# Kernel tuning notes

Measured on AMD Instinct MI355X. Metric: run time of the kernel, lower is better.

The kernel has to match this reference:

```python
import jax, jax.numpy as jnp
import numpy as np

T, D, H, E = 8192, 1024, 2048, 8


def setup_inputs() -> dict:
    key = jax.random.key(0)
    k1, k2, k3 = jax.random.split(key, 3)
    x = jax.random.normal(k1, (T, D), dtype=jnp.float32)
    # counts must sum to T; use a uniform split (reference handles any valid split)
    num_tokens_per_expert = jnp.full((E,), T // E, dtype=jnp.int32)
    w_up = jax.random.normal(k2, (E, H, D), dtype=jnp.float32) * (1.0 / np.sqrt(D))
    w_down = jax.random.normal(k3, (E, D, H), dtype=jnp.float32) * (1.0 / np.sqrt(H))
    return {"x": x, "num_tokens_per_expert": num_tokens_per_expert, "w_up": w_up, "w_down": w_down}


def reference(x, num_tokens_per_expert, w_up, w_down):
    """Grouped MoE expert MLP: per-expert  x @ w_up[e].T -> relu^2 -> @ w_down[e].T.
    Tokens are sorted by expert; counts encode the segment boundaries.
    Matches the CUDA path: bf16 compute for both GEMMs and the activation,
    final cast back to x.dtype.
    """
    n_tok = x.shape[0]
    n_exp = w_up.shape[0]
    # segment id per token from cumulative offsets (same as grouped_mm offs)
    offsets = jnp.cumsum(num_tokens_per_expert)  # (E,)
    expert_id = jnp.searchsorted(offsets, jnp.arange(n_tok), side="right")  # (T,)

    xb = x.astype(jnp.bfloat16)
    wu = w_up.astype(jnp.bfloat16)   # (E, H, D)
    wd = w_down.astype(jnp.bfloat16)  # (E, D, H)

    out = jnp.zeros((n_tok, x.shape[1]), dtype=jnp.bfloat16)
    # small fixed loop over experts; token dim fully vectorized
    for e in range(n_exp):
        h = jnp.maximum(xb @ wu[e].T, 0)          # (T, H) relu
        h = (h * h).astype(jnp.bfloat16)           # square, re-cast as original
        y = h @ wd[e].T                            # (T, D)
        out = out + jnp.where((expert_id == e)[:, None], y, jnp.bfloat16(0))
    return out.astype(x.dtype)
```

## Files before the change

### kernel.cpp

```cpp
#include <hip/hip_runtime.h>
#include <stdint.h>

constexpr int T_TOK = 8192;
constexpr int D_DIM = 1024;
constexpr int H_DIM = 2048;
constexpr int E_NUM = 8;

typedef __bf16 bf16x8 __attribute__((ext_vector_type(8)));
typedef float  f32x4  __attribute__((ext_vector_type(4)));

static __device__ __forceinline__ unsigned short f2bf(float f) {
  union { float f; unsigned u; } a; a.f = f;
  unsigned r = a.u + 0x7fffu + ((a.u >> 16) & 1u);
  return (unsigned short)(r >> 16);
}
static __device__ __forceinline__ float bf2f(unsigned short h) {
  union { unsigned u; float f; } a; a.u = ((unsigned)h) << 16;
  return a.f;
}

__global__ void cvt_f32_bf16(const float* __restrict__ src,
                             unsigned short* __restrict__ dst, int n4) {
  int i = blockIdx.x * blockDim.x + threadIdx.x;
  int stride = gridDim.x * blockDim.x;
  for (; i < n4; i += stride) {
    float4 v = reinterpret_cast<const float4*>(src)[i];
    ushort4 o;
    o.x = f2bf(v.x); o.y = f2bf(v.y); o.z = f2bf(v.z); o.w = f2bf(v.w);
    reinterpret_cast<ushort4*>(dst)[i] = o;
  }
}


#define FENCE() asm volatile("" ::: "memory")
#define BARRIER() do { FENCE(); __builtin_amdgcn_s_barrier(); FENCE(); } while (0)
#define WAIT_LGKM0() asm volatile("s_waitcnt lgkmcnt(0)" ::: "memory")
#define WAIT_VM(N) asm volatile("s_waitcnt vmcnt(%0)" :: "i"(N) : "memory")

template <int K_DIM, int N_DIM, int BN, bool RELU2>
__global__ __launch_bounds__(512, 2)
void gg8(const unsigned short* __restrict__ A,
         const unsigned short* __restrict__ Bw,
         const int* __restrict__ counts,
         void* __restrict__ Cout) {
  constexpr int BM = 256, BK = 64;
  constexpr int NT = K_DIM / BK;
  constexpr int NITER = NT / 2;
  constexpr int WNC = BN / 4;
  constexpr int NACC = WNC / 16;
  constexpr int NQN = NACC / 2;
  constexpr int BLOADS = (BN == 256) ? 2 : 1;
  constexpr int VN = 4 + BLOADS;

  const int tid  = threadIdx.x;
  const int wid  = tid >> 6;
  const int lane = tid & 63;
  const int wr   = wid >> 2;
  const int wc   = wid & 3;

  int t = blockIdx.x;
  int e = -1, rowBase = 0, rowsValid = 0;
  {
    int tiles = 0, off = 0;
#pragma unroll
    for (int i = 0; i < E_NUM; ++i) {
      int n  = counts[i];
      int nt = (n + BM - 1) / BM;
      if (e < 0 && t < tiles + nt) {
        e = i;
        int lt = t - tiles;
        rowBase   = off + lt * BM;
        rowsValid = n - lt * BM;
        if (rowsValid > BM) rowsValid = BM;
      }
      tiles += nt; off += n;
    }
  }
  if (e < 0) return;
  const int colBase = blockIdx.y * BN;

  __shared__ __align__(1024) char lds[(BM + BN) * BK * 2 * 2];
  auto ldsA = [&](int b) -> char* { return lds + b * (BM * 128); };
  auto ldsB = [&](int b) -> char* { return lds + 2 * (BM * 128) + b * (BN * 128); };

  const char* gA = (const char*)A + (size_t)rowBase * (K_DIM * 2);
  const char* gB = (const char*)(Bw + ((size_t)e * N_DIM + colBase) * K_DIM);

  const int lr8 = lane >> 3;
  const int gsw = (lane & 7) ^ lr8;

  auto stageA = [&](int buf, int alpha, int kt) {
#pragma unroll
    for (int j = 0; j < 2; ++j) {
      int bi   = j * 8 + wid;
      int row0 = (bi >> 3) * 128 + alpha * 64 + (bi & 7) * 8;
      int sr   = row0 + lr8;
      if (sr >= rowsValid) sr = rowsValid - 1;
      const char* src = gA + (size_t)sr * (K_DIM * 2) + (size_t)kt * 128 + gsw * 16;
      __builtin_amdgcn_global_load_lds(
          (const __attribute__((address_space(1))) void*)src,
          (__attribute__((address_space(3))) void*)(ldsA(buf) + row0 * 128),
          16, 0, 0);
    }
  };
  auto stageB = [&](int buf, int alpha, int kt) {
#pragma unroll
    for (int j = 0; j < BLOADS; ++j) {
      int bi   = j * 8 + wid;
      int row0 = (BN == 256) ? ((bi >> 2) * 64 + alpha * 32 + (bi & 3) * 8)
                             : ((bi >> 1) * 32 + alpha * 16 + (bi & 1) * 8);
      int sr   = row0 + lr8;
      const char* src = gB + (size_t)sr * (K_DIM * 2) + (size_t)kt * 128 + gsw * 16;
      __builtin_amdgcn_global_load_lds(
          (const __attribute__((address_space(1))) void*)src,
          (__attribute__((address_space(3))) void*)(ldsB(buf) + row0 * 128),
          16, 0, 0);
    }
  };

  const int rowLane = lane & 15;
  const int grpA    = lane >> 4;
  const int swzm    = lane & 7;

  bf16x8 aF[4][2];
  bf16x8 bF[2][NQN][2];
  f32x4  accC[8][NACC];
#pragma unroll
  for (int m = 0; m < 8; ++m)
#pragma unroll
    for (int n = 0; n < NACC; ++n) accC[m][n] = (f32x4){0.f, 0.f, 0.f, 0.f};

  auto readA = [&](int buf, int rh) {
    const char* base = ldsA(buf) + (wr * 128 + rh * 64 + rowLane) * 128;
#pragma unroll
    for (int m = 0; m < 4; ++m)
#pragma unroll
      for (int ks = 0; ks < 2; ++ks) {
        int g = (ks * 4 + grpA) ^ swzm;
        aF[m][ks] = *(const bf16x8*)(base + m * (16 * 128) + g * 16);
      }
  };
  auto readB = [&](int buf, int ch, bf16x8 (&dst)[NQN][2]) {
    const char* base = ldsB(buf) + (wc * WNC + ch * (WNC / 2) + rowLane) * 128;
#pragma unroll
    for (int n = 0; n < NQN; ++n)
#pragma unroll
      for (int ks = 0; ks < 2; ++ks) {
        int g = (ks * 4 + grpA) ^ swzm;
        dst[n][ks] = *(const bf16x8*)(base + n * (16 * 128) + g * 16);
      }
  };

#define MFMAQ(RH, BFA)                                                        \
  do {                                                                        \
    __builtin_amdgcn_s_setprio(1);                                            \
    _Pragma("unroll")                                                         \
    for (int m_ = 0; m_ < 4; ++m_) {                                          \
      _Pragma("unroll")                                                       \
      for (int n_ = 0; n_ < NQN; ++n_) {                                      \
        f32x4 c_ = accC[(RH) * 4 + m_][(CHIDX) * NQN + n_];                   \
        c_ = __builtin_amdgcn_mfma_f32_16x16x32_bf16(aF[m_][0], BFA[n_][0], c_, 0, 0, 0); \
        c_ = __builtin_amdgcn_mfma_f32_16x16x32_bf16(aF[m_][1], BFA[n_][1], c_, 0, 0, 0); \
        accC[(RH) * 4 + m_][(CHIDX) * NQN + n_] = c_;                         \
      }                                                                       \
    }                                                                         \
    __builtin_amdgcn_s_setprio(0);                                            \
  } while (0)

  stageA(0, 0, 0); stageB(0, 0, 0); stageA(0, 1, 0); stageB(0, 1, 0);
  stageA(1, 0, 1); stageB(1, 0, 1); stageA(1, 1, 1);
  WAIT_VM(VN);
  BARRIER();

  for (int it = 0; it < NITER; ++it) {
    const int t0  = 2 * it;
    const int kB1 = t0 + 1;
    const int kN0 = (t0 + 2 < NT) ? t0 + 2 : NT - 1;
    const int kN1 = (t0 + 3 < NT) ? t0 + 3 : NT - 1;

    readA(0, 0); readB(0, 0, bF[0]);
    stageB(1, 1, kB1);
    BARRIER(); WAIT_LGKM0();
#define CHIDX 0
    MFMAQ(0, bF[0]);
#undef CHIDX
    BARRIER();
    readB(0, 1, bF[1]);
    stageA(0, 0, kN0);
    BARRIER(); WAIT_LGKM0();
#define CHIDX 1
    MFMAQ(0, bF[1]);
#undef CHIDX
    BARRIER();
    readA(0, 1);
    stageB(0, 0, kN0);
    BARRIER(); WAIT_LGKM0();
#define CHIDX 1
    MFMAQ(1, bF[1]);
#undef CHIDX
    BARRIER();
    stageA(0, 1, kN0);
    WAIT_VM(VN);
    BARRIER();
#define CHIDX 0
    MFMAQ(1, bF[0]);
#undef CHIDX
    BARRIER();
    readA(1, 0); readB(1, 0, bF[0]);
    stageB(0, 1, kN0);
    BARRIER(); WAIT_LGKM0();
#define CHIDX 0
    MFMAQ(0, bF[0]);
#undef CHIDX
    BARRIER();
    readB(1, 1, bF[1]);
    stageA(1, 0, kN1);
    BARRIER(); WAIT_LGKM0();
#define CHIDX 1
    MFMAQ(0, bF[1]);
#undef CHIDX
    BARRIER();
    readA(1, 1);
    stageB(1, 0, kN1);
    BARRIER(); WAIT_LGKM0();
#define CHIDX 1
    MFMAQ(1, bF[1]);
#undef CHIDX
    BARRIER();
    stageA(1, 1, kN1);
    WAIT_VM(VN);
    BARRIER();
#define CHIDX 0
    MFMAQ(1, bF[0]);
#undef CHIDX
    BARRIER();
  }

  const int rB0 = wr * 128 + grpA * 4;
  const int cB0 = colBase + wc * WNC + rowLane;
#pragma unroll
  for (int m = 0; m < 8; ++m) {
#pragma unroll
    for (int n = 0; n < NACC; ++n) {
#pragma unroll
      for (int j = 0; j < 4; ++j) {
        int r = rB0 + m * 16 + j;
        if (r < rowsValid) {
          size_t idx = (size_t)(rowBase + r) * N_DIM + (cB0 + n * 16);
          float v = accC[m][n][j];
          if (RELU2) {
            v = v > 0.f ? v : 0.f;
            float hb = bf2f(f2bf(v));
            ((unsigned short*)Cout)[idx] = f2bf(hb * hb);
          } else {
            ((float*)Cout)[idx] = bf2f(f2bf(v));
          }
        }
      }
    }
  }
#undef MFMAQ
}

extern "C" void kernel_launch(void* const* d_in, const int* in_sizes, int n_in,
                              void* d_out, int out_size, void* d_ws, size_t ws_size,
                              hipStream_t stream) {
  const float* x   = (const float*)d_in[0];
  const int*   cnt = (const int*)d_in[1];
  const float* wu  = (const float*)d_in[2];
  const float* wd  = (const float*)d_in[3];
  float* out = (float*)d_out;
  char*  ws  = (char*)d_ws;

  unsigned short* xb   = (unsigned short*)(ws);
  unsigned short* wub  = (unsigned short*)(ws + (16u << 20));
  unsigned short* wdb  = (unsigned short*)(ws + (48u << 20));
  unsigned short* hbuf = (unsigned short*)(ws + (80u << 20));

  cvt_f32_bf16<<<2048, 256, 0, stream>>>(x,  xb,  T_TOK * D_DIM / 4);
  cvt_f32_bf16<<<2048, 256, 0, stream>>>(wu, wub, E_NUM * H_DIM * D_DIM / 4);
  cvt_f32_bf16<<<2048, 256, 0, stream>>>(wd, wdb, E_NUM * D_DIM * H_DIM / 4);

  gg8<D_DIM, H_DIM, 256, true ><<<dim3(40, H_DIM / 256), dim3(512), 0, stream>>>(
      xb, wub, cnt, (void*)hbuf);
  gg8<H_DIM, D_DIM, 128, false><<<dim3(40, D_DIM / 128), dim3(512), 0, stream>>>(
      hbuf, wdb, cnt, (void*)out);
}
```

Baseline: 129.2 us.

## Fuse fp32-to-bf16 weight conversion into grouped GEMM B-tile loads

Removes the two standalone weight conversion kernels. Both GEMMs now read fp32 weights directly into registers, convert them to bf16 and write the swizzled tiles into LDS. The main loop is restructured from a two-tile unrolled schedule into a single-tile double-buffered loop, with manual vmcnt waits and sched barriers interleaving the register-staged B loads. This saves a full pass over 128 MB of fp32 weights but doubles B-operand global traffic inside the GEMMs and adds VALU conversion work and register pressure.

```diff
diff --git a/kernel.cpp b/kernel.cpp
--- a/kernel.cpp
+++ b/kernel.cpp
@@ -8,6 +8,7 @@
 
 typedef __bf16 bf16x8 __attribute__((ext_vector_type(8)));
 typedef float  f32x4  __attribute__((ext_vector_type(4)));
+typedef unsigned int u32x4 __attribute__((ext_vector_type(4)));
 
 static __device__ __forceinline__ unsigned short f2bf(float f) {
   union { float f; unsigned u; } a; a.f = f;
@@ -31,26 +32,32 @@
   }
 }
 
-
 #define FENCE() asm volatile("" ::: "memory")
 #define BARRIER() do { FENCE(); __builtin_amdgcn_s_barrier(); FENCE(); } while (0)
 #define WAIT_LGKM0() asm volatile("s_waitcnt lgkmcnt(0)" ::: "memory")
 #define WAIT_VM(N) asm volatile("s_waitcnt vmcnt(%0)" :: "i"(N) : "memory")
+#define SCHED_FENCE() __builtin_amdgcn_sched_barrier(0)
+
+static __device__ __forceinline__ f32x4 gload4(const void* p) {
+  f32x4 r;
+  asm volatile("global_load_dwordx4 %0, %1, off" : "=v"(r) : "v"(p) : "memory");
+  return r;
+}
 
 template <int K_DIM, int N_DIM, int BN, bool RELU2>
 __global__ __launch_bounds__(512, 2)
 void gg8(const unsigned short* __restrict__ A,
-         const unsigned short* __restrict__ Bw,
+         const float* __restrict__ Bw,
          const int* __restrict__ counts,
          void* __restrict__ Cout) {
   constexpr int BM = 256, BK = 64;
   constexpr int NT = K_DIM / BK;
-  constexpr int NITER = NT / 2;
   constexpr int WNC = BN / 4;
   constexpr int NACC = WNC / 16;
   constexpr int NQN = NACC / 2;
-  constexpr int BLOADS = (BN == 256) ? 2 : 1;
-  constexpr int VN = 4 + BLOADS;
+  constexpr int BL = (BN == 256) ? 4 : 2;
+  constexpr int TSH = (BN == 256) ? 2 : 3;
+  constexpr int FPB = BL * 16;
 
   const int tid  = threadIdx.x;
   const int wid  = tid >> 6;
@@ -84,7 +91,10 @@
   auto ldsB = [&](int b) -> char* { return lds + 2 * (BM * 128) + b * (BN * 128); };
 
   const char* gA = (const char*)A + (size_t)rowBase * (K_DIM * 2);
-  const char* gB = (const char*)(Bw + ((size_t)e * N_DIM + colBase) * K_DIM);
+  const int  bRow0 = tid >> TSH;
+  const int  bByte = (tid & ((1 << TSH) - 1)) * FPB;
+  const char* gBbase = (const char*)Bw +
+      ((size_t)e * N_DIM + colBase) * (size_t)(K_DIM * 4);
 
   const int lr8 = lane >> 3;
   const int gsw = (lane & 7) ^ lr8;
@@ -103,18 +113,31 @@
           16, 0, 0);
     }
   };
-  auto stageB = [&](int buf, int alpha, int kt) {
-#pragma unroll
-    for (int j = 0; j < BLOADS; ++j) {
-      int bi   = j * 8 + wid;
-      int row0 = (BN == 256) ? ((bi >> 2) * 64 + alpha * 32 + (bi & 3) * 8)
-                             : ((bi >> 1) * 32 + alpha * 16 + (bi & 1) * 8);
-      int sr   = row0 + lr8;
-      const char* src = gB + (size_t)sr * (K_DIM * 2) + (size_t)kt * 128 + gsw * 16;
-      __builtin_amdgcn_global_load_lds(
-          (const __attribute__((address_space(1))) void*)src,
-          (__attribute__((address_space(3))) void*)(ldsB(buf) + row0 * 128),
-          16, 0, 0);
+
+  auto loadBhalf = [&](f32x4 (&q)[BL], int h, int kt) {
+    const char* s = gBbase + (size_t)(h * (BN / 2) + bRow0) * (K_DIM * 4)
+                  + (size_t)kt * 256 + bByte;
+#pragma unroll
+    for (int j = 0; j < BL; ++j) q[j] = gload4(s + j * 16);
+  };
+  auto writeBhalf = [&](int buf, const f32x4 (&q)[BL], int h) {
+    const int row = h * (BN / 2) + bRow0;
+    char* base = ldsB(buf) + row * 128;
+    const int rs = row & 7;
+#pragma unroll
+    for (int c = 0; c < BL / 2; ++c) {
+      u32x4 w;
+#pragma unroll
+      for (int k = 0; k < 2; ++k) {
+        const f32x4& v = q[c * 2 + k];
+#pragma unroll
+        for (int p = 0; p < 2; ++p) {
+          unsigned lo = f2bf(v[p * 2]), hi = f2bf(v[p * 2 + 1]);
+          w[k * 2 + p] = lo | (hi << 16);
+        }
+      }
+      int g = (BN == 256) ? (2 * (tid & 3) + c) : (tid & 7);
+      *reinterpret_cast<u32x4*>(base + (g ^ rs) * 16) = w;
     }
   };
 
@@ -123,7 +146,7 @@
   const int swzm    = lane & 7;
 
   bf16x8 aF[4][2];
-  bf16x8 bF[2][NQN][2];
+  bf16x8 bF0[NQN][2], bF1[NQN][2];
   f32x4  accC[8][NACC];
 #pragma unroll
   for (int m = 0; m < 8; ++m)
@@ -151,88 +174,65 @@
       }
   };
 
-#define MFMAQ(RH, BFA)                                                        \
+#define MFMAQ(RH, CH, BFA)                                                    \
   do {                                                                        \
     __builtin_amdgcn_s_setprio(1);                                            \
     _Pragma("unroll")                                                         \
     for (int m_ = 0; m_ < 4; ++m_) {                                          \
       _Pragma("unroll")                                                       \
       for (int n_ = 0; n_ < NQN; ++n_) {                                      \
-        f32x4 c_ = accC[(RH) * 4 + m_][(CHIDX) * NQN + n_];                   \
+        f32x4 c_ = accC[(RH) * 4 + m_][(CH) * NQN + n_];                      \
         c_ = __builtin_amdgcn_mfma_f32_16x16x32_bf16(aF[m_][0], BFA[n_][0], c_, 0, 0, 0); \
         c_ = __builtin_amdgcn_mfma_f32_16x16x32_bf16(aF[m_][1], BFA[n_][1], c_, 0, 0, 0); \
-        accC[(RH) * 4 + m_][(CHIDX) * NQN + n_] = c_;                         \
+        accC[(RH) * 4 + m_][(CH) * NQN + n_] = c_;                            \
       }                                                                       \
     }                                                                         \
     __builtin_amdgcn_s_setprio(0);                                            \
   } while (0)
 
-  stageA(0, 0, 0); stageB(0, 0, 0); stageA(0, 1, 0); stageB(0, 1, 0);
-  stageA(1, 0, 1); stageB(1, 0, 1); stageA(1, 1, 1);
-  WAIT_VM(VN);
+  f32x4 bq0[BL], bq1[BL];
+
+  loadBhalf(bq0, 0, 0);
+  loadBhalf(bq1, 1, 0);
+  stageA(0, 0, 0); stageA(0, 1, 0);
+  WAIT_VM(BL + 4);  SCHED_FENCE();  writeBhalf(0, bq0, 0);
+  WAIT_VM(4);       SCHED_FENCE();  writeBhalf(0, bq1, 1);
+  WAIT_VM(0); WAIT_LGKM0();
   BARRIER();
 
-  for (int it = 0; it < NITER; ++it) {
-    const int t0  = 2 * it;
-    const int kB1 = t0 + 1;
-    const int kN0 = (t0 + 2 < NT) ? t0 + 2 : NT - 1;
-    const int kN1 = (t0 + 3 < NT) ? t0 + 3 : NT - 1;
-
-    readA(0, 0); readB(0, 0, bF[0]);
-    stageB(1, 1, kB1);
-    BARRIER(); WAIT_LGKM0();
-#define CHIDX 0
-    MFMAQ(0, bF[0]);
-#undef CHIDX
-    BARRIER();
-    readB(0, 1, bF[1]);
-    stageA(0, 0, kN0);
-    BARRIER(); WAIT_LGKM0();
-#define CHIDX 1
-    MFMAQ(0, bF[1]);
-#undef CHIDX
-    BARRIER();
-    readA(0, 1);
-    stageB(0, 0, kN0);
-    BARRIER(); WAIT_LGKM0();
-#define CHIDX 1
-    MFMAQ(1, bF[1]);
-#undef CHIDX
-    BARRIER();
-    stageA(0, 1, kN0);
-    WAIT_VM(VN);
-    BARRIER();
-#define CHIDX 0
-    MFMAQ(1, bF[0]);
-#undef CHIDX
-    BARRIER();
-    readA(1, 0); readB(1, 0, bF[0]);
-    stageB(0, 1, kN0);
-    BARRIER(); WAIT_LGKM0();
-#define CHIDX 0
-    MFMAQ(0, bF[0]);
-#undef CHIDX
-    BARRIER();
-    readB(1, 1, bF[1]);
-    stageA(1, 0, kN1);
-    BARRIER(); WAIT_LGKM0();
-#define CHIDX 1
-    MFMAQ(0, bF[1]);
-#undef CHIDX
-    BARRIER();
-    readA(1, 1);
-    stageB(1, 0, kN1);
-    BARRIER(); WAIT_LGKM0();
-#define CHIDX 1
-    MFMAQ(1, bF[1]);
-#undef CHIDX
-    BARRIER();
-    stageA(1, 1, kN1);
-    WAIT_VM(VN);
-    BARRIER();
-#define CHIDX 0
-    MFMAQ(1, bF[0]);
-#undef CHIDX
+  for (int t2 = 0; t2 < NT; ++t2) {
+    const int cur = t2 & 1, nxt = cur ^ 1;
+    const int ktn = (t2 + 1 < NT) ? t2 + 1 : NT - 1;
+
+    loadBhalf(bq0, 0, ktn);
+    readA(cur, 0); readB(cur, 0, bF0);
+    BARRIER(); WAIT_LGKM0();
+    MFMAQ(0, 0, bF0);
+    BARRIER();
+
+    loadBhalf(bq1, 1, ktn);
+    stageA(nxt, 0, ktn);
+    readB(cur, 1, bF1);
+    BARRIER(); WAIT_LGKM0();
+    MFMAQ(0, 1, bF1);
+    WAIT_VM(2 * BL + 2);
+    BARRIER();
+
+    WAIT_VM(BL + 2);
+    SCHED_FENCE();
+    writeBhalf(nxt, bq0, 0);
+    stageA(nxt, 1, ktn);
+    readA(cur, 1);
+    BARRIER(); WAIT_LGKM0();
+    MFMAQ(1, 1, bF1);
+    BARRIER();
+
+    WAIT_VM(4);
+    SCHED_FENCE();
+    writeBhalf(nxt, bq1, 1);
+    WAIT_VM(2);
+    BARRIER(); WAIT_LGKM0();
+    MFMAQ(1, 0, bF0);
     BARRIER();
   }
 
@@ -273,16 +273,12 @@
   char*  ws  = (char*)d_ws;
 
   unsigned short* xb   = (unsigned short*)(ws);
-  unsigned short* wub  = (unsigned short*)(ws + (16u << 20));
-  unsigned short* wdb  = (unsigned short*)(ws + (48u << 20));
-  unsigned short* hbuf = (unsigned short*)(ws + (80u << 20));
-
-  cvt_f32_bf16<<<2048, 256, 0, stream>>>(x,  xb,  T_TOK * D_DIM / 4);
-  cvt_f32_bf16<<<2048, 256, 0, stream>>>(wu, wub, E_NUM * H_DIM * D_DIM / 4);
-  cvt_f32_bf16<<<2048, 256, 0, stream>>>(wd, wdb, E_NUM * D_DIM * H_DIM / 4);
+  unsigned short* hbuf = (unsigned short*)(ws + (16u << 20));
+
+  cvt_f32_bf16<<<2048, 256, 0, stream>>>(x, xb, T_TOK * D_DIM / 4);
 
   gg8<D_DIM, H_DIM, 256, true ><<<dim3(40, H_DIM / 256), dim3(512), 0, stream>>>(
-      xb, wub, cnt, (void*)hbuf);
+      xb, wu, cnt, (void*)hbuf);
   gg8<H_DIM, D_DIM, 128, false><<<dim3(40, D_DIM / 128), dim3(512), 0, stream>>>(
-      hbuf, wdb, cnt, (void*)out);
-}
+      hbuf, wd, cnt, (void*)out);
+}
```

Measured after the change: 126.9 us. About the same (-1.8%).

## Fuse fp32-to-bf16 weight conversion into GEMM B-tile loads

Applied to the files above, without the earlier changes.

Drops the two standalone weight conversion kernels. The grouped GEMMs now stream fp32 weights straight into LDS with an XOR swizzle and convert them to bf16 when reading fragments. Both GEMMs use BN=128 with a linearized, column-grouped block order. This removes a full read and write pass over the weights, but doubles B-tile load bytes and LDS footprint and adds conversion ALU work inside the main loop.

```diff
diff --git a/kernel.cpp b/kernel.cpp
--- a/kernel.cpp
+++ b/kernel.cpp
@@ -13,10 +13,6 @@
   union { float f; unsigned u; } a; a.f = f;
   unsigned r = a.u + 0x7fffu + ((a.u >> 16) & 1u);
   return (unsigned short)(r >> 16);
-}
-static __device__ __forceinline__ float bf2f(unsigned short h) {
-  union { unsigned u; float f; } a; a.u = ((unsigned)h) << 16;
-  return a.f;
 }
 
 __global__ void cvt_f32_bf16(const float* __restrict__ src,
@@ -31,26 +27,22 @@
   }
 }
 
-
 #define FENCE() asm volatile("" ::: "memory")
 #define BARRIER() do { FENCE(); __builtin_amdgcn_s_barrier(); FENCE(); } while (0)
 #define WAIT_LGKM0() asm volatile("s_waitcnt lgkmcnt(0)" ::: "memory")
 #define WAIT_VM(N) asm volatile("s_waitcnt vmcnt(%0)" :: "i"(N) : "memory")
 
-template <int K_DIM, int N_DIM, int BN, bool RELU2>
+template <int K_DIM, int N_DIM, bool RELU2>
 __global__ __launch_bounds__(512, 2)
-void gg8(const unsigned short* __restrict__ A,
-         const unsigned short* __restrict__ Bw,
+void ggf(const unsigned short* __restrict__ A,
+         const float* __restrict__ Bw,
          const int* __restrict__ counts,
          void* __restrict__ Cout) {
-  constexpr int BM = 256, BK = 64;
+  constexpr int BM = 256, BK = 64, BN = 128;
   constexpr int NT = K_DIM / BK;
   constexpr int NITER = NT / 2;
-  constexpr int WNC = BN / 4;
-  constexpr int NACC = WNC / 16;
-  constexpr int NQN = NACC / 2;
-  constexpr int BLOADS = (BN == 256) ? 2 : 1;
-  constexpr int VN = 4 + BLOADS;
+  constexpr int NCOLT = N_DIM / BN;
+  constexpr int VN = 6;
 
   const int tid  = threadIdx.x;
   const int wid  = tid >> 6;
@@ -58,7 +50,12 @@
   const int wr   = wid >> 2;
   const int wc   = wid & 3;
 
-  int t = blockIdx.x;
+  const int id = blockIdx.x + gridDim.x * blockIdx.y;
+  int ct, rt;
+  if (NCOLT == 16) { ct = (id & 7) | (((id >> 3) & 1) << 3); rt = id >> 4; }
+  else             { ct = id & 7;                            rt = id >> 3; }
+
+  int t = rt;
   int e = -1, rowBase = 0, rowsValid = 0;
   {
     int tiles = 0, off = 0;
@@ -77,17 +74,17 @@
     }
   }
   if (e < 0) return;
-  const int colBase = blockIdx.y * BN;
-
-  __shared__ __align__(1024) char lds[(BM + BN) * BK * 2 * 2];
+  const int colBase = ct * BN;
+
+  __shared__ __align__(1024) char lds[2 * BM * 128 + 2 * BN * 256];
   auto ldsA = [&](int b) -> char* { return lds + b * (BM * 128); };
-  auto ldsB = [&](int b) -> char* { return lds + 2 * (BM * 128) + b * (BN * 128); };
+  auto ldsB = [&](int b) -> char* { return lds + 2 * (BM * 128) + b * (BN * 256); };
 
   const char* gA = (const char*)A + (size_t)rowBase * (K_DIM * 2);
-  const char* gB = (const char*)(Bw + ((size_t)e * N_DIM + colBase) * K_DIM);
+  const char* gB = (const char*)Bw + ((size_t)e * N_DIM + colBase) * (size_t)(K_DIM * 4);
 
   const int lr8 = lane >> 3;
-  const int gsw = (lane & 7) ^ lr8;
+  const int gswA = (lane & 7) ^ lr8;
 
   auto stageA = [&](int buf, int alpha, int kt) {
 #pragma unroll
@@ -96,39 +93,39 @@
       int row0 = (bi >> 3) * 128 + alpha * 64 + (bi & 7) * 8;
       int sr   = row0 + lr8;
       if (sr >= rowsValid) sr = rowsValid - 1;
-      const char* src = gA + (size_t)sr * (K_DIM * 2) + (size_t)kt * 128 + gsw * 16;
+      const char* src = gA + (size_t)sr * (K_DIM * 2) + (size_t)kt * 128 + gswA * 16;
       __builtin_amdgcn_global_load_lds(
           (const __attribute__((address_space(1))) void*)src,
           (__attribute__((address_space(3))) void*)(ldsA(buf) + row0 * 128),
           16, 0, 0);
     }
   };
+
   auto stageB = [&](int buf, int alpha, int kt) {
 #pragma unroll
-    for (int j = 0; j < BLOADS; ++j) {
-      int bi   = j * 8 + wid;
-      int row0 = (BN == 256) ? ((bi >> 2) * 64 + alpha * 32 + (bi & 3) * 8)
-                             : ((bi >> 1) * 32 + alpha * 16 + (bi & 1) * 8);
-      int sr   = row0 + lr8;
-      const char* src = gB + (size_t)sr * (K_DIM * 2) + (size_t)kt * 128 + gsw * 16;
+    for (int j = 0; j < 2; ++j) {
+      int row0u = alpha * 64 + j * 32 + wid * 4;
+      int row   = row0u + (lane >> 4);
+      int srcg  = (lane & 15) ^ (row & 15);
+      const char* src = gB + (size_t)row * (K_DIM * 4) + (size_t)kt * 256 + srcg * 16;
       __builtin_amdgcn_global_load_lds(
           (const __attribute__((address_space(1))) void*)src,
-          (__attribute__((address_space(3))) void*)(ldsB(buf) + row0 * 128),
+          (__attribute__((address_space(3))) void*)(ldsB(buf) + row0u * 256),
           16, 0, 0);
     }
   };
 
   const int rowLane = lane & 15;
   const int grpA    = lane >> 4;
-  const int swzm    = lane & 7;
+  const int swzmA   = lane & 7;
 
   bf16x8 aF[4][2];
-  bf16x8 bF[2][NQN][2];
-  f32x4  accC[8][NACC];
+  bf16x8 bF0[2], bF1[2];
+  f32x4  accC[8][2];
 #pragma unroll
   for (int m = 0; m < 8; ++m)
 #pragma unroll
-    for (int n = 0; n < NACC; ++n) accC[m][n] = (f32x4){0.f, 0.f, 0.f, 0.f};
+    for (int n = 0; n < 2; ++n) accC[m][n] = (f32x4){0.f, 0.f, 0.f, 0.f};
 
   auto readA = [&](int buf, int rh) {
     const char* base = ldsA(buf) + (wr * 128 + rh * 64 + rowLane) * 128;
@@ -136,33 +133,35 @@
     for (int m = 0; m < 4; ++m)
 #pragma unroll
       for (int ks = 0; ks < 2; ++ks) {
-        int g = (ks * 4 + grpA) ^ swzm;
+        int g = (ks * 4 + grpA) ^ swzmA;
         aF[m][ks] = *(const bf16x8*)(base + m * (16 * 128) + g * 16);
       }
   };
-  auto readB = [&](int buf, int ch, bf16x8 (&dst)[NQN][2]) {
-    const char* base = ldsB(buf) + (wc * WNC + ch * (WNC / 2) + rowLane) * 128;
-#pragma unroll
-    for (int n = 0; n < NQN; ++n)
-#pragma unroll
-      for (int ks = 0; ks < 2; ++ks) {
-        int g = (ks * 4 + grpA) ^ swzm;
-        dst[n][ks] = *(const bf16x8*)(base + n * (16 * 128) + g * 16);
-      }
-  };
-
-#define MFMAQ(RH, BFA)                                                        \
+  auto readB = [&](int buf, int ch, bf16x8 (&dst)[2]) {
+    const char* base = ldsB(buf) + (wc * 32 + ch * 16 + rowLane) * 256;
+#pragma unroll
+    for (int ks = 0; ks < 2; ++ks) {
+      f32x4 v0 = *(const f32x4*)(base + (((ks * 8 + grpA * 2 + 0) ^ rowLane) * 16));
+      f32x4 v1 = *(const f32x4*)(base + (((ks * 8 + grpA * 2 + 1) ^ rowLane) * 16));
+      union { __bf16 b[8]; bf16x8 v; } u;
+#pragma unroll
+      for (int p = 0; p < 4; ++p) {
+        u.b[p]     = (__bf16)v0[p];
+        u.b[4 + p] = (__bf16)v1[p];
+      }
+      dst[ks] = u.v;
+    }
+  };
+
+#define MFMAQ2(RH, CH, BFA)                                                   \
   do {                                                                        \
     __builtin_amdgcn_s_setprio(1);                                            \
     _Pragma("unroll")                                                         \
     for (int m_ = 0; m_ < 4; ++m_) {                                          \
-      _Pragma("unroll")                                                       \
-      for (int n_ = 0; n_ < NQN; ++n_) {                                      \
-        f32x4 c_ = accC[(RH) * 4 + m_][(CHIDX) * NQN + n_];                   \
-        c_ = __builtin_amdgcn_mfma_f32_16x16x32_bf16(aF[m_][0], BFA[n_][0], c_, 0, 0, 0); \
-        c_ = __builtin_amdgcn_mfma_f32_16x16x32_bf16(aF[m_][1], BFA[n_][1], c_, 0, 0, 0); \
-        accC[(RH) * 4 + m_][(CHIDX) * NQN + n_] = c_;                         \
-      }                                                                       \
+      f32x4 c_ = accC[(RH) * 4 + m_][(CH)];                                   \
+      c_ = __builtin_amdgcn_mfma_f32_16x16x32_bf16(aF[m_][0], BFA[0], c_, 0, 0, 0); \
+      c_ = __builtin_amdgcn_mfma_f32_16x16x32_bf16(aF[m_][1], BFA[1], c_, 0, 0, 0); \
+      accC[(RH) * 4 + m_][(CH)] = c_;                                         \
     }                                                                         \
     __builtin_amdgcn_s_setprio(0);                                            \
   } while (0)
@@ -178,70 +177,55 @@
     const int kN0 = (t0 + 2 < NT) ? t0 + 2 : NT - 1;
     const int kN1 = (t0 + 3 < NT) ? t0 + 3 : NT - 1;
 
-    readA(0, 0); readB(0, 0, bF[0]);
+    readA(0, 0); readB(0, 0, bF0);
     stageB(1, 1, kB1);
     BARRIER(); WAIT_LGKM0();
-#define CHIDX 0
-    MFMAQ(0, bF[0]);
-#undef CHIDX
-    BARRIER();
-    readB(0, 1, bF[1]);
+    MFMAQ2(0, 0, bF0);
+    BARRIER();
+    readB(0, 1, bF1);
     stageA(0, 0, kN0);
     BARRIER(); WAIT_LGKM0();
-#define CHIDX 1
-    MFMAQ(0, bF[1]);
-#undef CHIDX
+    MFMAQ2(0, 1, bF1);
     BARRIER();
     readA(0, 1);
     stageB(0, 0, kN0);
     BARRIER(); WAIT_LGKM0();
-#define CHIDX 1
-    MFMAQ(1, bF[1]);
-#undef CHIDX
+    MFMAQ2(1, 1, bF1);
     BARRIER();
     stageA(0, 1, kN0);
     WAIT_VM(VN);
     BARRIER();
-#define CHIDX 0
-    MFMAQ(1, bF[0]);
-#undef CHIDX
-    BARRIER();
-    readA(1, 0); readB(1, 0, bF[0]);
+    MFMAQ2(1, 0, bF0);
+    BARRIER();
+    readA(1, 0); readB(1, 0, bF0);
     stageB(0, 1, kN0);
     BARRIER(); WAIT_LGKM0();
-#define CHIDX 0
-    MFMAQ(0, bF[0]);
-#undef CHIDX
-    BARRIER();
-    readB(1, 1, bF[1]);
+    MFMAQ2(0, 0, bF0);
+    BARRIER();
+    readB(1, 1, bF1);
     stageA(1, 0, kN1);
     BARRIER(); WAIT_LGKM0();
-#define CHIDX 1
-    MFMAQ(0, bF[1]);
-#undef CHIDX
+    MFMAQ2(0, 1, bF1);
     BARRIER();
     readA(1, 1);
     stageB(1, 0, kN1);
     BARRIER(); WAIT_LGKM0();
-#define CHIDX 1
-    MFMAQ(1, bF[1]);
-#undef CHIDX
+    MFMAQ2(1, 1, bF1);
     BARRIER();
     stageA(1, 1, kN1);
     WAIT_VM(VN);
     BARRIER();
-#define CHIDX 0
-    MFMAQ(1, bF[0]);
-#undef CHIDX
-    BARRIER();
-  }
+    MFMAQ2(1, 0, bF0);
+    BARRIER();
+  }
+#undef MFMAQ2
 
   const int rB0 = wr * 128 + grpA * 4;
-  const int cB0 = colBase + wc * WNC + rowLane;
+  const int cB0 = colBase + wc * 32 + rowLane;
 #pragma unroll
   for (int m = 0; m < 8; ++m) {
 #pragma unroll
-    for (int n = 0; n < NACC; ++n) {
+    for (int n = 0; n < 2; ++n) {
 #pragma unroll
       for (int j = 0; j < 4; ++j) {
         int r = rB0 + m * 16 + j;
@@ -249,17 +233,16 @@
           size_t idx = (size_t)(rowBase + r) * N_DIM + (cB0 + n * 16);
           float v = accC[m][n][j];
           if (RELU2) {
-            v = v > 0.f ? v : 0.f;
-            float hb = bf2f(f2bf(v));
-            ((unsigned short*)Cout)[idx] = f2bf(hb * hb);
+            float rl = v > 0.f ? v : 0.f;
+            float hf = (float)(__bf16)rl;
+            ((__bf16*)Cout)[idx] = (__bf16)(hf * hf);
           } else {
-            ((float*)Cout)[idx] = bf2f(f2bf(v));
+            ((float*)Cout)[idx] = (float)(__bf16)v;
           }
         }
       }
     }
   }
-#undef MFMAQ
 }
 
 extern "C" void kernel_launch(void* const* d_in, const int* in_sizes, int n_in,
@@ -273,16 +256,12 @@
   char*  ws  = (char*)d_ws;
 
   unsigned short* xb   = (unsigned short*)(ws);
-  unsigned short* wub  = (unsigned short*)(ws + (16u << 20));
-  unsigned short* wdb  = (unsigned short*)(ws + (48u << 20));
-  unsigned short* hbuf = (unsigned short*)(ws + (80u << 20));
-
-  cvt_f32_bf16<<<2048, 256, 0, stream>>>(x,  xb,  T_TOK * D_DIM / 4);
-  cvt_f32_bf16<<<2048, 256, 0, stream>>>(wu, wub, E_NUM * H_DIM * D_DIM / 4);
-  cvt_f32_bf16<<<2048, 256, 0, stream>>>(wd, wdb, E_NUM * D_DIM * H_DIM / 4);
-
-  gg8<D_DIM, H_DIM, 256, true ><<<dim3(40, H_DIM / 256), dim3(512), 0, stream>>>(
-      xb, wub, cnt, (void*)hbuf);
-  gg8<H_DIM, D_DIM, 128, false><<<dim3(40, D_DIM / 128), dim3(512), 0, stream>>>(
-      hbuf, wdb, cnt, (void*)out);
-}
+  unsigned short* hbuf = (unsigned short*)(ws + (16u << 20));
+
+  cvt_f32_bf16<<<2048, 256, 0, stream>>>(x, xb, T_TOK * D_DIM / 4);
+
+  ggf<D_DIM, H_DIM, true ><<<dim3(40, H_DIM / 128), dim3(512), 0, stream>>>(
+      xb, wu, cnt, (void*)hbuf);
+  ggf<H_DIM, D_DIM, false><<<dim3(40, D_DIM / 128), dim3(512), 0, stream>>>(
+      hbuf, wd, cnt, (void*)out);
+}
```

Result: faster. 122.0 us (-5.6%).
